# Performance work log

Measured on AMD Instinct MI355X. Metric: run time of the kernel, lower is better.

## Reference

```python
import jax, jax.numpy as jnp
import numpy as np

B, L, K, D = 1024, 8, 16, 64
_KSCALE = 1.0 / np.sqrt(K * D)  # keep channel roughly norm-preserving over layers


def setup_inputs() -> dict:
    key = jax.random.key(0)
    k1, k2, k3, k4 = jax.random.split(key, 4)
    state_re = jax.random.normal(k1, (B, D, D), dtype=jnp.float32)
    state_im = jax.random.normal(k2, (B, D, D), dtype=jnp.float32)
    kraus_re = jax.random.normal(k3, (L, K, D, D), dtype=jnp.float32) * _KSCALE
    kraus_im = jax.random.normal(k4, (L, K, D, D), dtype=jnp.float32) * _KSCALE
    return {"state_re": state_re, "state_im": state_im,
            "kraus_re": kraus_re, "kraus_im": kraus_im}


def reference(state_re, state_im, kraus_re, kraus_im):
    # rho: [B, d, d] complex density matrices; kraus: [L, K, d, d]
    rho = (state_re + 1j * state_im).astype(jnp.complex64)
    kraus = (kraus_re + 1j * kraus_im).astype(jnp.complex64)

    def layer_step(rho, Kl):
        # Kl: [K, d, d]. output_state = sum_k  K_k @ rho @ K_k^dagger
        tmp = jnp.einsum('kij,bjl->kbil', Kl, rho)            # K_k @ rho
        rho_new = jnp.einsum('kbil,kml->bim', tmp, Kl.conj())  # (...) @ K_k^dagger, summed over k
        return rho_new, None

    rho, _ = jax.lax.scan(layer_step, rho, kraus)
    # return real/imag stacked as float32: [2, B, d, d]
    return jnp.stack([rho.real, rho.imag])
```

## Files before the change

### kernel.cpp

```cpp
#include <hip/hip_runtime.h>
#include <hip/hip_fp16.h>

#define D 64
#define NKR 16
#define NB 1024
#define NL 8

typedef __attribute__((ext_vector_type(8))) _Float16 half8;
typedef __attribute__((ext_vector_type(16))) float f32x16;
typedef __attribute__((ext_vector_type(4))) int i32x4;

static __device__ __forceinline__ half8 neg8(half8 x) {
    i32x4 u = __builtin_bit_cast(i32x4, x);
    u = u ^ (int)0x80008000;
    return __builtin_bit_cast(half8, u);
}

static __device__ __forceinline__ unsigned pkrtz(float a, float b) {
    auto h = __builtin_amdgcn_cvt_pkrtz(a, b);
    return __builtin_bit_cast(unsigned, h);
}

static __device__ __forceinline__ void plswap(unsigned &a, unsigned &b) {
    asm volatile("v_permlane32_swap_b32 %0, %1" : "+v"(a), "+v"(b));
}

union Pack4 { _Float16 h[4]; uint2 u; };
union H8 { unsigned u[4]; uint2 v[2]; half8 h; };

#define GLDS16(gp, lp) \
    __builtin_amdgcn_global_load_lds((const __attribute__((address_space(1))) void*)(gp), \
                                     (__attribute__((address_space(3))) void*)(lp), 16, 0, 0)

#define MFMA __builtin_amdgcn_mfma_f32_32x32x16_f16

__global__ void kconv_kernel(const float* __restrict__ re, const float* __restrict__ im,
                             _Float16* __restrict__ out) {
    int plane = blockIdx.y;
    int idx = blockIdx.x * blockDim.x + threadIdx.x;
    const float* src = plane ? im : re;
    float4 v = ((const float4*)src)[idx];
    int e = idx * 4;
    int lk = e >> 12;
    int rem = e & 4095;
    int row = rem >> 6, col = rem & 63;
    int grp = (col >> 2) ^ (row & 15);
    Pack4 p;
    p.h[0] = (_Float16)v.x; p.h[1] = (_Float16)v.y;
    p.h[2] = (_Float16)v.z; p.h[3] = (_Float16)v.w;
    *(uint2*)(out + ((size_t)lk * 2 + plane) * 4096 + row * 64 + grp * 4) = p.u;
}

__global__ void sconv_kernel(const float* __restrict__ re, const float* __restrict__ im,
                             _Float16* __restrict__ out) {
    __shared__ float tile[64][65];
    int b = blockIdx.x;
    int t = threadIdx.x;
    for (int plane = 0; plane < 2; ++plane) {
        const float* src = (plane ? im : re) + (size_t)b * 4096;
        __syncthreads();
        #pragma unroll
        for (int i = 0; i < 16; ++i) {
            int e = t + 256 * i;
            tile[e >> 6][e & 63] = src[e];
        }
        __syncthreads();
        _Float16* o = out + ((size_t)b * 2 + plane) * 4096;
        #pragma unroll
        for (int i = 0; i < 16; ++i) {
            int e = t + 256 * i;
            o[e] = (_Float16)tile[e & 63][e >> 6];
        }
    }
}

static __device__ __forceinline__ void exchange(const f32x16 &dd, half8 &f0, half8 &f1) {
    unsigned A0 = pkrtz(dd[0],  dd[1]),  B0 = pkrtz(dd[2],  dd[3]);
    unsigned A1 = pkrtz(dd[4],  dd[5]),  B1 = pkrtz(dd[6],  dd[7]);
    unsigned A2 = pkrtz(dd[8],  dd[9]),  B2 = pkrtz(dd[10], dd[11]);
    unsigned A3 = pkrtz(dd[12], dd[13]), B3 = pkrtz(dd[14], dd[15]);
    plswap(A0, A1);
    plswap(B0, B1);
    plswap(A2, A3);
    plswap(B2, B3);
    H8 h0; h0.u[0] = A0; h0.u[1] = B0; h0.u[2] = A1; h0.u[3] = B1; f0 = h0.h;
    H8 h1; h1.u[0] = A2; h1.u[1] = B2; h1.u[2] = A3; h1.u[3] = B3; f1 = h1.h;
}

template<int IT>
static __device__ __forceinline__ void kstep(
    const _Float16* __restrict__ KB,
    const half8 (&a1re)[2][4], const half8 (&a1im)[2][4],
    f32x16 (&accRe)[2], f32x16 (&accIm)[2],
    int l31, int hl)
{
    const int rx = l31 & 15;

    half8 bre0[4], bim0[4], bimn[4];
    {
        const int base = (32 * IT + l31) * 64;
        #pragma unroll
        for (int ks = 0; ks < 4; ++ks) {
            const int g = 4 * ks + 2 * hl;
            const int p = ((g ^ rx) << 2);
            const int q = (((g + 1) ^ rx) << 2);
            H8 t;
            t.v[0] = *(const uint2*)&KB[base + p];
            t.v[1] = *(const uint2*)&KB[base + q];
            bre0[ks] = t.h;
            t.v[0] = *(const uint2*)&KB[4096 + base + p];
            t.v[1] = *(const uint2*)&KB[4096 + base + q];
            bim0[ks] = t.h;
            bimn[ks] = neg8(bim0[ks]);
        }
    }

    half8 af_re[4], af_im[4];
    #pragma unroll
    for (int lh = 0; lh < 2; ++lh) {
        f32x16 ddre, ddim;
        #pragma unroll
        for (int i = 0; i < 16; ++i) { ddre[i] = 0.f; ddim[i] = 0.f; }
        #pragma unroll
        for (int ks = 0; ks < 4; ++ks) {
            ddre = MFMA(a1re[lh][ks], bre0[ks], ddre, 0, 0, 0);
            ddre = MFMA(a1im[lh][ks], bimn[ks], ddre, 0, 0, 0);
            ddim = MFMA(a1re[lh][ks], bim0[ks], ddim, 0, 0, 0);
            ddim = MFMA(a1im[lh][ks], bre0[ks], ddim, 0, 0, 0);
        }
        exchange(ddre, af_re[2 * lh], af_re[2 * lh + 1]);
        exchange(ddim, af_im[2 * lh], af_im[2 * lh + 1]);
    }

    #pragma unroll
    for (int ks = 0; ks < 4; ++ks) {
        half8 an = neg8(af_re[ks]);
        accRe[IT] = MFMA(af_re[ks], bre0[ks], accRe[IT], 0, 0, 0);
        accRe[IT] = MFMA(af_im[ks], bim0[ks], accRe[IT], 0, 0, 0);
        accIm[IT] = MFMA(af_im[ks], bre0[ks], accIm[IT], 0, 0, 0);
        accIm[IT] = MFMA(an,        bim0[ks], accIm[IT], 0, 0, 0);
    }

    {
        const int base = (32 * (1 - IT) + l31) * 64;
        #pragma unroll
        for (int ks = 0; ks < 4; ++ks) {
            const int g = 4 * ks + 2 * hl;
            const int p = ((g ^ rx) << 2);
            const int q = (((g + 1) ^ rx) << 2);
            H8 t;
            t.v[0] = *(const uint2*)&KB[base + p];
            t.v[1] = *(const uint2*)&KB[base + q];
            half8 br = t.h;
            t.v[0] = *(const uint2*)&KB[4096 + base + p];
            t.v[1] = *(const uint2*)&KB[4096 + base + q];
            half8 bi = t.h;
            half8 an = neg8(af_re[ks]);
            accRe[1 - IT] = MFMA(af_re[ks], br, accRe[1 - IT], 0, 0, 0);
            accRe[1 - IT] = MFMA(af_im[ks], bi, accRe[1 - IT], 0, 0, 0);
            accIm[1 - IT] = MFMA(af_im[ks], br, accIm[1 - IT], 0, 0, 0);
            accIm[1 - IT] = MFMA(an,        bi, accIm[1 - IT], 0, 0, 0);
        }
    }
}

__global__ __launch_bounds__(128, 2) void layer_kernel(
    const _Float16* __restrict__ rho_in,
    _Float16* __restrict__ rho_out,
    float* __restrict__ final_out,
    const _Float16* __restrict__ kraus,
    int last)
{
    __shared__ __align__(16) _Float16 Klds[2][2 * D * D];

    const int b    = blockIdx.x;
    const int t    = threadIdx.x;
    const int wv   = t >> 6;
    const int lane = t & 63;
    const int l31  = lane & 31;
    const int hl   = lane >> 5;

    half8 a1re[2][4], a1im[2][4];
    {
        const _Float16* rb = rho_in + (size_t)b * 2 * D * D;
        #pragma unroll
        for (int lh = 0; lh < 2; ++lh) {
            const int row = 32 * lh + l31;
            #pragma unroll
            for (int ks = 0; ks < 4; ++ks) {
                const int col = 16 * ks + 8 * hl;
                a1re[lh][ks] = *(const half8*)(rb + row * D + col);
                a1im[lh][ks] = *(const half8*)(rb + D * D + row * D + col);
            }
        }
    }

    {
        const char* kb = (const char*)kraus;
        const int off = wv * 8192;
        #pragma unroll
        for (int rr = 0; rr < 8; ++rr)
            GLDS16(kb + off + rr * 1024 + lane * 16, (char*)&Klds[0][0] + off + rr * 1024);
    }

    f32x16 accRe[2], accIm[2];
    #pragma unroll
    for (int mt = 0; mt < 2; ++mt)
        #pragma unroll
        for (int i = 0; i < 16; ++i) { accRe[mt][i] = 0.f; accIm[mt][i] = 0.f; }

    __syncthreads();

    #pragma unroll 1
    for (int k = 0; k < NKR; ++k) {
        if (k + 1 < NKR) {
            const char* kb = (const char*)(kraus + (size_t)(k + 1) * 2 * D * D);
            const int off = wv * 8192;
            #pragma unroll
            for (int rr = 0; rr < 8; ++rr)
                GLDS16(kb + off + rr * 1024 + lane * 16,
                       (char*)&Klds[(k + 1) & 1][0] + off + rr * 1024);
        }
        const _Float16* KB = &Klds[0][0] + (k & 1) * (2 * D * D);
        if (wv == 0) kstep<0>(KB, a1re, a1im, accRe, accIm, l31, hl);
        else         kstep<1>(KB, a1re, a1im, accRe, accIm, l31, hl);
        __syncthreads();
    }

    const int IT = wv;
    if (!last) {
        _Float16* ob = rho_out + (size_t)b * 2 * D * D;
        #pragma unroll
        for (int mt = 0; mt < 2; ++mt) {
            const int m = 32 * mt + l31;
            #pragma unroll
            for (int g = 0; g < 4; ++g) {
                Pack4 pr, pi;
                #pragma unroll
                for (int j = 0; j < 4; ++j) {
                    pr.h[j] = (_Float16)accRe[mt][4 * g + j];
                    pi.h[j] = (_Float16)accIm[mt][4 * g + j];
                }
                const int i0 = 32 * IT + 8 * g + 4 * hl;
                *(uint2*)(ob + m * D + i0)         = pr.u;
                *(uint2*)(ob + D * D + m * D + i0) = pi.u;
            }
        }
    } else {
        float* o0 = final_out + (size_t)b * 4096;
        float* o1 = final_out + (size_t)(NB + b) * 4096;
        #pragma unroll
        for (int mt = 0; mt < 2; ++mt) {
            const int m = 32 * mt + l31;
            #pragma unroll
            for (int g = 0; g < 4; ++g) {
                #pragma unroll
                for (int j = 0; j < 4; ++j) {
                    const int i = 32 * IT + 8 * g + 4 * hl + j;
                    o0[i * D + m] = accRe[mt][4 * g + j];
                    o1[i * D + m] = accIm[mt][4 * g + j];
                }
            }
        }
    }
}

extern "C" void kernel_launch(void* const* d_in, const int* in_sizes, int n_in,
                              void* d_out, int out_size, void* d_ws, size_t ws_size,
                              hipStream_t stream) {
    const float* state_re = (const float*)d_in[0];
    const float* state_im = (const float*)d_in[1];
    const float* kraus_re = (const float*)d_in[2];
    const float* kraus_im = (const float*)d_in[3];

    _Float16* kraus_h = (_Float16*)d_ws;
    _Float16* bufA = (_Float16*)d_out;
    _Float16* bufB = (_Float16*)((char*)d_out + (size_t)NB * 2 * D * D * sizeof(_Float16));
    float* fout = (float*)d_out;

    kconv_kernel<<<dim3(512, 2), 256, 0, stream>>>(kraus_re, kraus_im, kraus_h);
    sconv_kernel<<<NB, 256, 0, stream>>>(state_re, state_im, bufA);

    for (int l = 0; l < NL; ++l) {
        const _Float16* in = (l & 1) ? bufB : bufA;
        _Float16* out      = (l & 1) ? bufA : bufB;
        layer_kernel<<<NB, 128, 0, stream>>>(in, out, fout,
                                             kraus_h + (size_t)l * NKR * 2 * D * D,
                                             (l == NL - 1) ? 1 : 0);
    }
}
```

Measured before the change: 572.8 us.

## Pre-swizzle Kraus and state into MFMA fragment layout, drop LDS staging

```diff
diff --git a/kernel.cpp b/kernel.cpp
--- a/kernel.cpp
+++ b/kernel.cpp
@@ -28,11 +28,8 @@
 union Pack4 { _Float16 h[4]; uint2 u; };
 union H8 { unsigned u[4]; uint2 v[2]; half8 h; };
 
-#define GLDS16(gp, lp) \
-    __builtin_amdgcn_global_load_lds((const __attribute__((address_space(1))) void*)(gp), \
-                                     (__attribute__((address_space(3))) void*)(lp), 16, 0, 0)
-
 #define MFMA __builtin_amdgcn_mfma_f32_32x32x16_f16
+
 
 __global__ void kconv_kernel(const float* __restrict__ re, const float* __restrict__ im,
                              _Float16* __restrict__ out) {
@@ -44,11 +41,14 @@
     int lk = e >> 12;
     int rem = e & 4095;
     int row = rem >> 6, col = rem & 63;
-    int grp = (col >> 2) ^ (row & 15);
+    int ihalf = row >> 5, r31 = row & 31;
+    int ks = col >> 4, hl2 = (col >> 3) & 1, c = col & 7;
     Pack4 p;
     p.h[0] = (_Float16)v.x; p.h[1] = (_Float16)v.y;
     p.h[2] = (_Float16)v.z; p.h[3] = (_Float16)v.w;
-    *(uint2*)(out + ((size_t)lk * 2 + plane) * 4096 + row * 64 + grp * 4) = p.u;
+    size_t off = (size_t)(lk * 2 + plane) * 4096 + ihalf * 2048
+               + (2 * ks + hl2) * 256 + r31 * 8 + c;
+    *(uint2*)(out + off) = p.u;
 }
 
 __global__ void sconv_kernel(const float* __restrict__ re, const float* __restrict__ im,
@@ -68,8 +68,11 @@
         _Float16* o = out + ((size_t)b * 2 + plane) * 4096;
         #pragma unroll
         for (int i = 0; i < 16; ++i) {
-            int e = t + 256 * i;
-            o[e] = (_Float16)tile[e & 63][e >> 6];
+            int oi = t + 256 * i;
+            int lh = oi >> 11, slot = (oi >> 8) & 7, r = (oi >> 3) & 31, c = oi & 7;
+            int col = 16 * (slot >> 1) + 8 * (slot & 1) + c;
+            int row = 32 * lh + r;
+            o[oi] = (_Float16)tile[col][row];
         }
     }
 }
@@ -89,94 +92,91 @@
 
 template<int IT>
 static __device__ __forceinline__ void kstep(
-    const _Float16* __restrict__ KB,
+    const _Float16* __restrict__ kb,
     const half8 (&a1re)[2][4], const half8 (&a1im)[2][4],
     f32x16 (&accRe)[2], f32x16 (&accIm)[2],
-    int l31, int hl)
+    int lane)
 {
-    const int rx = l31 & 15;
-
-    half8 bre0[4], bim0[4], bimn[4];
-    {
-        const int base = (32 * IT + l31) * 64;
-        #pragma unroll
-        for (int ks = 0; ks < 4; ++ks) {
-            const int g = 4 * ks + 2 * hl;
-            const int p = ((g ^ rx) << 2);
-            const int q = (((g + 1) ^ rx) << 2);
-            H8 t;
-            t.v[0] = *(const uint2*)&KB[base + p];
-            t.v[1] = *(const uint2*)&KB[base + q];
-            bre0[ks] = t.h;
-            t.v[0] = *(const uint2*)&KB[4096 + base + p];
-            t.v[1] = *(const uint2*)&KB[4096 + base + q];
-            bim0[ks] = t.h;
-            bimn[ks] = neg8(bim0[ks]);
-        }
-    }
-
-    half8 af_re[4], af_im[4];
+    const _Float16* bo = kb + IT * 2048;
+    const _Float16* bx = kb + (1 - IT) * 2048;
+
+    half8 bre[4], bim[4];
+    #pragma unroll
+    for (int ks = 0; ks < 4; ++ks) {
+        bre[ks] = *(const half8*)(bo + ks * 512 + lane * 8);
+        bim[ks] = *(const half8*)(bo + 4096 + ks * 512 + lane * 8);
+    }
+
     #pragma unroll
     for (int lh = 0; lh < 2; ++lh) {
         f32x16 ddre, ddim;
         #pragma unroll
         for (int i = 0; i < 16; ++i) { ddre[i] = 0.f; ddim[i] = 0.f; }
+        __builtin_amdgcn_s_setprio(1);
         #pragma unroll
         for (int ks = 0; ks < 4; ++ks) {
-            ddre = MFMA(a1re[lh][ks], bre0[ks], ddre, 0, 0, 0);
-            ddre = MFMA(a1im[lh][ks], bimn[ks], ddre, 0, 0, 0);
-            ddim = MFMA(a1re[lh][ks], bim0[ks], ddim, 0, 0, 0);
-            ddim = MFMA(a1im[lh][ks], bre0[ks], ddim, 0, 0, 0);
-        }
-        exchange(ddre, af_re[2 * lh], af_re[2 * lh + 1]);
-        exchange(ddim, af_im[2 * lh], af_im[2 * lh + 1]);
-    }
-
-    #pragma unroll
-    for (int ks = 0; ks < 4; ++ks) {
-        half8 an = neg8(af_re[ks]);
-        accRe[IT] = MFMA(af_re[ks], bre0[ks], accRe[IT], 0, 0, 0);
-        accRe[IT] = MFMA(af_im[ks], bim0[ks], accRe[IT], 0, 0, 0);
-        accIm[IT] = MFMA(af_im[ks], bre0[ks], accIm[IT], 0, 0, 0);
-        accIm[IT] = MFMA(an,        bim0[ks], accIm[IT], 0, 0, 0);
-    }
-
-    {
-        const int base = (32 * (1 - IT) + l31) * 64;
-        #pragma unroll
-        for (int ks = 0; ks < 4; ++ks) {
-            const int g = 4 * ks + 2 * hl;
-            const int p = ((g ^ rx) << 2);
-            const int q = (((g + 1) ^ rx) << 2);
-            H8 t;
-            t.v[0] = *(const uint2*)&KB[base + p];
-            t.v[1] = *(const uint2*)&KB[base + q];
-            half8 br = t.h;
-            t.v[0] = *(const uint2*)&KB[4096 + base + p];
-            t.v[1] = *(const uint2*)&KB[4096 + base + q];
-            half8 bi = t.h;
-            half8 an = neg8(af_re[ks]);
-            accRe[1 - IT] = MFMA(af_re[ks], br, accRe[1 - IT], 0, 0, 0);
-            accRe[1 - IT] = MFMA(af_im[ks], bi, accRe[1 - IT], 0, 0, 0);
-            accIm[1 - IT] = MFMA(af_im[ks], br, accIm[1 - IT], 0, 0, 0);
-            accIm[1 - IT] = MFMA(an,        bi, accIm[1 - IT], 0, 0, 0);
-        }
-    }
-}
-
-__global__ __launch_bounds__(128, 2) void layer_kernel(
+            half8 bn = neg8(bim[ks]);
+            ddre = MFMA(a1re[lh][ks], bre[ks], ddre, 0, 0, 0);
+            ddre = MFMA(a1im[lh][ks], bn,      ddre, 0, 0, 0);
+            ddim = MFMA(a1re[lh][ks], bim[ks], ddim, 0, 0, 0);
+            ddim = MFMA(a1im[lh][ks], bre[ks], ddim, 0, 0, 0);
+        }
+        __builtin_amdgcn_s_setprio(0);
+
+        half8 br2[2], bi2[2];
+        #pragma unroll
+        for (int c = 0; c < 2; ++c) {
+            const int ks = 2 * lh + c;
+            br2[c] = *(const half8*)(bx + ks * 512 + lane * 8);
+            bi2[c] = *(const half8*)(bx + 4096 + ks * 512 + lane * 8);
+        }
+
+        half8 fre0, fre1, fim0, fim1;
+        exchange(ddre, fre0, fre1);
+        exchange(ddim, fim0, fim1);
+
+        #pragma unroll
+        for (int c = 0; c < 2; ++c) {
+            const int ks = 2 * lh + c;
+            half8 afre = c ? fre1 : fre0;
+            half8 afim = c ? fim1 : fim0;
+            half8 an  = neg8(afre);
+            __builtin_amdgcn_s_setprio(1);
+            accRe[IT]     = MFMA(afre, bre[ks], accRe[IT], 0, 0, 0);
+            accRe[IT]     = MFMA(afim, bim[ks], accRe[IT], 0, 0, 0);
+            accIm[IT]     = MFMA(afim, bre[ks], accIm[IT], 0, 0, 0);
+            accIm[IT]     = MFMA(an,   bim[ks], accIm[IT], 0, 0, 0);
+            accRe[1 - IT] = MFMA(afre, br2[c],  accRe[1 - IT], 0, 0, 0);
+            accRe[1 - IT] = MFMA(afim, bi2[c],  accRe[1 - IT], 0, 0, 0);
+            accIm[1 - IT] = MFMA(afim, br2[c],  accIm[1 - IT], 0, 0, 0);
+            accIm[1 - IT] = MFMA(an,   bi2[c],  accIm[1 - IT], 0, 0, 0);
+            __builtin_amdgcn_s_setprio(0);
+        }
+    }
+}
+
+template<int IT>
+static __device__ __forceinline__ void run_layer(
+    const _Float16* __restrict__ kraus,
+    const half8 (&a1re)[2][4], const half8 (&a1im)[2][4],
+    f32x16 (&accRe)[2], f32x16 (&accIm)[2],
+    int lane)
+{
+    #pragma unroll 1
+    for (int k = 0; k < NKR; ++k)
+        kstep<IT>(kraus + (size_t)k * 8192, a1re, a1im, accRe, accIm, lane);
+}
+
+__global__ __launch_bounds__(64, 2) void layer_kernel(
     const _Float16* __restrict__ rho_in,
     _Float16* __restrict__ rho_out,
     float* __restrict__ final_out,
     const _Float16* __restrict__ kraus,
     int last)
 {
-    __shared__ __align__(16) _Float16 Klds[2][2 * D * D];
-
     const int b    = blockIdx.x;
-    const int t    = threadIdx.x;
-    const int wv   = t >> 6;
-    const int lane = t & 63;
+    const int IT   = blockIdx.y;
+    const int lane = threadIdx.x;
     const int l31  = lane & 31;
     const int hl   = lane >> 5;
 
@@ -184,23 +184,12 @@
     {
         const _Float16* rb = rho_in + (size_t)b * 2 * D * D;
         #pragma unroll
-        for (int lh = 0; lh < 2; ++lh) {
-            const int row = 32 * lh + l31;
+        for (int lh = 0; lh < 2; ++lh)
             #pragma unroll
             for (int ks = 0; ks < 4; ++ks) {
-                const int col = 16 * ks + 8 * hl;
-                a1re[lh][ks] = *(const half8*)(rb + row * D + col);
-                a1im[lh][ks] = *(const half8*)(rb + D * D + row * D + col);
+                a1re[lh][ks] = *(const half8*)(rb + lh * 2048 + ks * 512 + lane * 8);
+                a1im[lh][ks] = *(const half8*)(rb + 4096 + lh * 2048 + ks * 512 + lane * 8);
             }
-        }
-    }
-
-    {
-        const char* kb = (const char*)kraus;
-        const int off = wv * 8192;
-        #pragma unroll
-        for (int rr = 0; rr < 8; ++rr)
-            GLDS16(kb + off + rr * 1024 + lane * 16, (char*)&Klds[0][0] + off + rr * 1024);
     }
 
     f32x16 accRe[2], accIm[2];
@@ -209,30 +198,13 @@
         #pragma unroll
         for (int i = 0; i < 16; ++i) { accRe[mt][i] = 0.f; accIm[mt][i] = 0.f; }
 
-    __syncthreads();
-
-    #pragma unroll 1
-    for (int k = 0; k < NKR; ++k) {
-        if (k + 1 < NKR) {
-            const char* kb = (const char*)(kraus + (size_t)(k + 1) * 2 * D * D);
-            const int off = wv * 8192;
-            #pragma unroll
-            for (int rr = 0; rr < 8; ++rr)
-                GLDS16(kb + off + rr * 1024 + lane * 16,
-                       (char*)&Klds[(k + 1) & 1][0] + off + rr * 1024);
-        }
-        const _Float16* KB = &Klds[0][0] + (k & 1) * (2 * D * D);
-        if (wv == 0) kstep<0>(KB, a1re, a1im, accRe, accIm, l31, hl);
-        else         kstep<1>(KB, a1re, a1im, accRe, accIm, l31, hl);
-        __syncthreads();
-    }
-
-    const int IT = wv;
+    if (IT == 0) run_layer<0>(kraus, a1re, a1im, accRe, accIm, lane);
+    else         run_layer<1>(kraus, a1re, a1im, accRe, accIm, lane);
+
     if (!last) {
         _Float16* ob = rho_out + (size_t)b * 2 * D * D;
         #pragma unroll
         for (int mt = 0; mt < 2; ++mt) {
-            const int m = 32 * mt + l31;
             #pragma unroll
             for (int g = 0; g < 4; ++g) {
                 Pack4 pr, pi;
@@ -241,9 +213,9 @@
                     pr.h[j] = (_Float16)accRe[mt][4 * g + j];
                     pi.h[j] = (_Float16)accIm[mt][4 * g + j];
                 }
-                const int i0 = 32 * IT + 8 * g + 4 * hl;
-                *(uint2*)(ob + m * D + i0)         = pr.u;
-                *(uint2*)(ob + D * D + m * D + i0) = pi.u;
+                const int off = mt * 2048 + (4 * IT + g) * 256 + l31 * 8 + 4 * hl;
+                *(uint2*)(ob + off)        = pr.u;
+                *(uint2*)(ob + 4096 + off) = pi.u;
             }
         }
     } else {
@@ -284,8 +256,8 @@
     for (int l = 0; l < NL; ++l) {
         const _Float16* in = (l & 1) ? bufB : bufA;
         _Float16* out      = (l & 1) ? bufA : bufB;
-        layer_kernel<<<NB, 128, 0, stream>>>(in, out, fout,
-                                             kraus_h + (size_t)l * NKR * 2 * D * D,
-                                             (l == NL - 1) ? 1 : 0);
-    }
-}
+        layer_kernel<<<dim3(NB, 2), 64, 0, stream>>>(in, out, fout,
+                                                     kraus_h + (size_t)l * NKR * 2 * D * D,
+                                                     (l == NL - 1) ? 1 : 0);
+    }
+}
```

New measurement: 544.7 us. 1.05x faster.
